# Performance work log

Measured on AMD Instinct MI355X. Metric: run time of the kernel, lower is better.

Reference implementation:

```python
import jax, jax.numpy as jnp
import numpy as np

NEG_INF = -1e9


def setup_inputs() -> dict:
    B, S, D = 4, 2048, 1024
    key = jax.random.key(0)
    ks = jax.random.split(key, 10)
    sc = 1.0 / np.sqrt(D)
    return {
        "batch": jax.random.normal(ks[0], (B, S, D), jnp.float32),
        "padding_mask": jax.random.randint(ks[1], (B, S), 0, 2) > 0,
        "Wq": jax.random.normal(ks[2], (D, D), jnp.float32) * sc,
        "bq": jnp.zeros((D,), jnp.float32),
        "Wk": jax.random.normal(ks[3], (D, D), jnp.float32) * sc,
        "bk": jnp.zeros((D,), jnp.float32),
        "Wv": jax.random.normal(ks[4], (D, D), jnp.float32) * sc,
        "bv": jnp.zeros((D,), jnp.float32),
        "Wo": jax.random.normal(ks[5], (D, D), jnp.float32) * sc,
        "bo": jnp.zeros((D,), jnp.float32),
        "num_heads": 16,
    }


def _split_heads(x, H):
    B, S, D = x.shape
    return x.reshape(B, S, H, D // H).transpose(0, 2, 1, 3)  # [B,H,S,hd]


def reference(batch, padding_mask, Wq, bq, Wk, bk, Wv, bv, Wo, bo, num_heads):
    B, S, D = batch.shape
    H = num_heads
    q = _split_heads(batch @ Wq + bq, H)  # [B,H,S,hd]
    k = _split_heads(batch @ Wk + bk, H)
    v = _split_heads(batch @ Wv + bv, H)
    # tf.keras.layers.Attention default: unscaled dot-product scores
    scores = jnp.einsum("bhqd,bhkd->bhqk", q, k)
    kmask = padding_mask[:, None, None, :]  # value/key mask -> masks score columns
    scores = jnp.where(kmask, scores, NEG_INF)
    probs = jax.nn.softmax(scores, axis=-1)
    ctx = jnp.einsum("bhqk,bhkd->bhqd", probs, v)
    # query mask zeroes padded query positions (tf Attention behavior)
    ctx = ctx * padding_mask[:, None, :, None].astype(ctx.dtype)
    ctx = ctx.transpose(0, 2, 1, 3).reshape(B, S, D)
    return ctx @ Wo + bo
```

## Files before the change

### kernel.cpp

```cpp
#include <hip/hip_runtime.h>


#define Bb 4
#define Ss 2048
#define Dd 1024
#define Hh 16
#define SZt 8388608

typedef short bf16x8 __attribute__((ext_vector_type(8)));
typedef _Float16 f16x8 __attribute__((ext_vector_type(8)));
typedef float f32x4 __attribute__((ext_vector_type(4)));
typedef float f32x16 __attribute__((ext_vector_type(16)));
typedef unsigned int u32x4 __attribute__((ext_vector_type(4)));
typedef unsigned short u16;

__device__ __forceinline__ float bf2f(u16 u) {
    return __builtin_bit_cast(float, ((unsigned)u) << 16);
}
__device__ __forceinline__ u16 f2bf(float f) {
    unsigned u = __builtin_bit_cast(unsigned, f);
    unsigned r = 0x7FFFu + ((u >> 16) & 1u);
    return (u16)((u + r) >> 16);
}
__device__ __forceinline__ u16 f2h(float f) {
    _Float16 h = (_Float16)f;
    return __builtin_bit_cast(u16, h);
}
__device__ __forceinline__ bf16x8 ldfrag(const u16* p) {
    return __builtin_bit_cast(bf16x8, *(const uint4*)p);
}
__device__ __forceinline__ f16x8 ldfragh(const u16* p) {
    return __builtin_bit_cast(f16x8, *(const uint4*)p);
}
__device__ __forceinline__ f32x4 mfma16h(f16x8 a, f16x8 b, f32x4 c) {
    return __builtin_amdgcn_mfma_f32_16x16x32_f16(a, b, c, 0, 0, 0);
}
__device__ __forceinline__ f32x16 mfma32(bf16x8 a, bf16x8 b, f32x16 c) {
    return __builtin_amdgcn_mfma_f32_32x32x16_bf16(a, b, c, 0, 0, 0);
}
__device__ __forceinline__ f32x16 mfma32h(f16x8 a, f16x8 b, f32x16 c) {
    return __builtin_amdgcn_mfma_f32_32x32x16_f16(a, b, c, 0, 0, 0);
}
__device__ __forceinline__ unsigned cvt_pk_bf16(float a, float b) {
    unsigned r;
    asm("v_cvt_pk_bf16_f32 %0, %1, %2" : "=v"(r) : "v"(a), "v"(b));
    return r;
}
__device__ __forceinline__ void gl2lds16(const u16* g, u16* l) {
    __builtin_amdgcn_global_load_lds(
        (const __attribute__((address_space(1))) u16*)g,
        (__attribute__((address_space(3))) u16*)l, 16, 0, 0);
}

__global__ void normalize_mask(const unsigned char* __restrict__ raw, float* __restrict__ out,
                               float* __restrict__ cnt, int n) {
    __shared__ int flags;
    __shared__ float scnt[Bb];
    if (threadIdx.x == 0) flags = 0;
    if (threadIdx.x < Bb) scnt[threadIdx.x] = 0.f;
    __syncthreads();
    int f = 0;
    for (int i = threadIdx.x; i < n; i += blockDim.x) {
        unsigned char c = raw[i];
        if ((i & 3) != 0 && c) f |= 1;
        if ((i & 3) == 1 && c >= 2) f |= 2;
        if ((i & 3) == 3 && c >= 2) f |= 4;
    }
    if (f) atomicOr(&flags, f);
    __syncthreads();
    int fl = flags;
    int layout;
    if (!(fl & 1)) layout = 0;
    else if (fl & 2) layout = 2;
    else if (fl & 4) layout = 3;
    else layout = 1;
    for (int i = threadIdx.x; i < n; i += blockDim.x) {
        int v;
        if (layout == 0)      v = ((const int*)raw)[i];
        else if (layout == 1) v = raw[i];
        else if (layout == 2) v = ((const u16*)raw)[i] != 0;
        else                  v = ((const unsigned*)raw)[i] != 0;
        out[i] = (v != 0) ? 1.0f : 0.0f;
        if (v == 0) atomicAdd(&scnt[i >> 11], 1.0f);
    }
    __syncthreads();
    if (threadIdx.x < Bb) cnt[threadIdx.x] = scnt[threadIdx.x];
}

__global__ void concat_bias(const float* __restrict__ a, const float* __restrict__ b,
                            const float* __restrict__ c, float* __restrict__ o) {
    int i = blockIdx.x * 256 + threadIdx.x;
    o[i] = (i < 1024) ? a[i] : ((i < 2048) ? b[i - 1024] : c[i - 2048]);
}

__global__ __launch_bounds__(256) void convert_xh(const float* __restrict__ X,
                                                  u16* __restrict__ Xh) {
    size_t i = ((size_t)blockIdx.x * 256 + threadIdx.x) * 4;
    float4 v = *(const float4*)(X + i);
    u16 h0 = f2h(v.x), h1 = f2h(v.y), h2 = f2h(v.z), h3 = f2h(v.w);
    uint2 ph = { (unsigned)h0 | ((unsigned)h1 << 16), (unsigned)h2 | ((unsigned)h3 << 16) };
    *(uint2*)(Xh + i) = ph;
}

__global__ __launch_bounds__(256) void transpose_wh(const float* __restrict__ W, u16* __restrict__ Wt) {
    __shared__ float t[32][33];
    const int tx = threadIdx.x, ty = threadIdx.y;
    const int n0 = blockIdx.x * 32, k0 = blockIdx.y * 32;
    #pragma unroll
    for (int i = 0; i < 4; i++)
        t[ty + i * 8][tx] = W[(size_t)(k0 + ty + i * 8) * Dd + n0 + tx];
    __syncthreads();
    #pragma unroll
    for (int i = 0; i < 4; i++)
        Wt[(size_t)(n0 + ty + i * 8) * Dd + k0 + tx] = f2h(t[tx][ty + i * 8]);
}
__global__ __launch_bounds__(256) void transpose_w(const float* __restrict__ W, u16* __restrict__ Wt) {
    __shared__ float t[32][33];
    const int tx = threadIdx.x, ty = threadIdx.y;
    const int n0 = blockIdx.x * 32, k0 = blockIdx.y * 32;
    #pragma unroll
    for (int i = 0; i < 4; i++)
        t[ty + i * 8][tx] = W[(size_t)(k0 + ty + i * 8) * Dd + n0 + tx];
    __syncthreads();
    #pragma unroll
    for (int i = 0; i < 4; i++)
        Wt[(size_t)(n0 + ty + i * 8) * Dd + k0 + tx] = f2bf(t[tx][ty + i * 8]);
}

__global__ __launch_bounds__(256) void gemm_qkv(
    const u16* __restrict__ Ah, const u16* __restrict__ Wcat, const float* __restrict__ bcat,
    const float* __restrict__ mnorm,
    u16* __restrict__ Qb, u16* __restrict__ Kb, u16* __restrict__ Vt)
{
    __shared__ u16 Ahs[128][64];
    __shared__ u16 Bs[128][64];
    const int tid = threadIdx.x, lane = tid & 63, wave = tid >> 6;
    const int wm = wave >> 1, wn = wave & 1;
    const int bm = blockIdx.y * 128, bn = blockIdx.x * 128;
    const bool isQ = (bn < 1024);
    const int l15 = lane & 15, lq = lane >> 4;
    const int sr = wave * 32 + (lane >> 3);
    const int sc = (lane & 7) * 8;
    const u16* agp = Ah + (size_t)(bm + sr) * Dd + sc;
    const u16* bgp = Wcat + (size_t)(bn + sr) * Dd + sc;

    f32x4 acc[4][4] = {};

    for (int k0 = 0; k0 < Dd; k0 += 64) {
        __syncthreads();
        #pragma unroll
        for (int j = 0; j < 4; j++) {
            gl2lds16(agp + k0 + (size_t)j * 8 * Dd, &Ahs[wave * 32 + j * 8][0]);
            gl2lds16(bgp + k0 + (size_t)j * 8 * Dd, &Bs[wave * 32 + j * 8][0]);
        }
        __syncthreads();
        #pragma unroll
        for (int kf = 0; kf < 2; kf++) {
            f16x8 b[4], a[4];
            #pragma unroll
            for (int nt = 0; nt < 4; nt++)
                b[nt] = ldfragh(&Bs[wn * 64 + nt * 16 + l15][kf * 32 + lq * 8]);
            #pragma unroll
            for (int mt = 0; mt < 4; mt++)
                a[mt] = ldfragh(&Ahs[wm * 64 + mt * 16 + l15][kf * 32 + lq * 8]);
            #pragma unroll
            for (int mt = 0; mt < 4; mt++)
                #pragma unroll
                for (int nt = 0; nt < 4; nt++)
                    acc[mt][nt] = mfma16h(a[mt], b[nt], acc[mt][nt]);
        }
    }
    const float LOG2E = 1.44269504088896f;
    float bv[4];
    #pragma unroll
    for (int nt = 0; nt < 4; nt++) bv[nt] = bcat[bn + wn * 64 + nt * 16 + l15];
    #pragma unroll
    for (int mt = 0; mt < 4; mt++) {
        int r0 = bm + wm * 64 + mt * 16 + lq * 4;
        float mk[4];
        if (!isQ) {
            #pragma unroll
            for (int rr = 0; rr < 4; rr++) mk[rr] = mnorm[r0 + rr];
        }
        #pragma unroll
        for (int nt = 0; nt < 4; nt++) {
            int col = bn + wn * 64 + nt * 16 + l15;
            if (col < 1024) {
                #pragma unroll
                for (int rr = 0; rr < 4; rr++)
                    Qb[(size_t)(r0 + rr) * Dd + col] = f2h((acc[mt][nt][rr] + bv[nt]) * LOG2E);
            } else if (col < 2048) {
                int c2 = col - 1024;
                #pragma unroll
                for (int rr = 0; rr < 4; rr++)
                    Kb[(size_t)(r0 + rr) * Dd + c2] = f2h((acc[mt][nt][rr] + bv[nt]) * mk[rr]);
            } else {
                int c2 = col - 2048;
                int hh = c2 >> 6, dd = c2 & 63, b_ = r0 >> 11, s0 = r0 & 2047;
                u16 e0 = f2bf((acc[mt][nt][0] + bv[nt]) * mk[0]);
                u16 e1 = f2bf((acc[mt][nt][1] + bv[nt]) * mk[1]);
                u16 e2 = f2bf((acc[mt][nt][2] + bv[nt]) * mk[2]);
                u16 e3 = f2bf((acc[mt][nt][3] + bv[nt]) * mk[3]);
                uint2 pk = { (unsigned)e0 | ((unsigned)e1 << 16), (unsigned)e2 | ((unsigned)e3 << 16) };
                *(uint2*)(Vt + (size_t)((b_ * Hh + hh) * 64 + dd) * Ss + s0) = pk;
            }
        }
    }
}

__global__ __launch_bounds__(256) void gemm_out(
    const u16* __restrict__ Ah, const u16* __restrict__ Wt,
    const float* __restrict__ bias, float* __restrict__ Cout)
{
    __shared__ u16 Ahs[128][64];
    __shared__ u16 Bs[128][64];
    const int tid = threadIdx.x, lane = tid & 63, wave = tid >> 6;
    const int wm = wave >> 1, wn = wave & 1;
    const int bm = blockIdx.y * 128, bn = blockIdx.x * 128;
    const int l15 = lane & 15, lq = lane >> 4;
    const int sr = wave * 32 + (lane >> 3);
    const int sc = (lane & 7) * 8;
    const u16* agp = Ah + (size_t)(bm + sr) * Dd + sc;
    const u16* bgp = Wt + (size_t)(bn + sr) * Dd + sc;

    f32x4 acc[4][4] = {};

    for (int k0 = 0; k0 < Dd; k0 += 64) {
        __syncthreads();
        #pragma unroll
        for (int j = 0; j < 4; j++) {
            gl2lds16(agp + k0 + (size_t)j * 8 * Dd, &Ahs[wave * 32 + j * 8][0]);
            gl2lds16(bgp + k0 + (size_t)j * 8 * Dd, &Bs[wave * 32 + j * 8][0]);
        }
        __syncthreads();
        #pragma unroll
        for (int kf = 0; kf < 2; kf++) {
            bf16x8 b[4], a[4];
            #pragma unroll
            for (int nt = 0; nt < 4; nt++)
                b[nt] = ldfrag(&Bs[wn * 64 + nt * 16 + l15][kf * 32 + lq * 8]);
            #pragma unroll
            for (int mt = 0; mt < 4; mt++)
                a[mt] = ldfrag(&Ahs[wm * 64 + mt * 16 + l15][kf * 32 + lq * 8]);
            #pragma unroll
            for (int mt = 0; mt < 4; mt++)
                #pragma unroll
                for (int nt = 0; nt < 4; nt++)
                    acc[mt][nt] = __builtin_amdgcn_mfma_f32_16x16x32_bf16(a[mt], b[nt], acc[mt][nt], 0, 0, 0);
        }
    }
    float bv[4];
    #pragma unroll
    for (int nt = 0; nt < 4; nt++) bv[nt] = bias[bn + wn * 64 + nt * 16 + l15];
    #pragma unroll
    for (int mt = 0; mt < 4; mt++) {
        int r0 = bm + wm * 64 + mt * 16 + lq * 4;
        #pragma unroll
        for (int nt = 0; nt < 4; nt++) {
            int col = bn + wn * 64 + nt * 16 + l15;
            #pragma unroll
            for (int rr = 0; rr < 4; rr++)
                Cout[(size_t)(r0 + rr) * Dd + col] = acc[mt][nt][rr] + bv[nt];
        }
    }
}

__global__ __launch_bounds__(512, 4) void attn_mfma(
    u16* qctx, const u16* __restrict__ Kb, const u16* __restrict__ Vt,
    const float* __restrict__ maskf, const float* __restrict__ cntp)
{
    __shared__ u16 Ks[64][72];
    __shared__ u16 Vs[64][72];
    __shared__ float li_s[8][32];
    const int tid = threadIdx.x, lane = tid & 63, wave = tid >> 6;
    const int l31 = lane & 31, hi = lane >> 5;
    const int bh = blockIdx.x, h = bh & 15, b = bh >> 4;
    const int q0 = blockIdx.y * 256;

    f16x8 qa[4];
    {
        const u16* qp = qctx + (size_t)(b * Ss + q0 + wave * 32 + l31) * Dd + h * 64 + hi * 8;
        #pragma unroll
        for (int kf = 0; kf < 4; kf++) qa[kf] = ldfragh(qp + kf * 16);
    }

    const int srow = tid >> 3, scol = (tid & 7) * 8;
    const u16* kgsrc = Kb + (size_t)(b * Ss + srow) * Dd + h * 64 + scol;
    const u16* vgsrc = Vt + (size_t)((b * Hh + h) * 64 + srow) * Ss + scol;
    u16* kdst = &Ks[srow][scol];
    u16* vdst = &Vs[srow][scol];

    f32x16 acc0 = {}, acc1 = {};
    float li = 0.f;

    uint4 kreg = *(const uint4*)kgsrc;
    uint4 vreg = *(const uint4*)vgsrc;

    for (int k0 = 0; k0 < Ss; k0 += 64) {
        __syncthreads();
        *(uint4*)kdst = kreg;
        *(uint4*)vdst = vreg;
        __syncthreads();
        int k0n = (k0 + 64 < Ss) ? k0 + 64 : 0;
        kreg = *(const uint4*)(kgsrc + (size_t)k0n * Dd);
        vreg = *(const uint4*)(vgsrc + k0n);

        #pragma unroll
        for (int nt = 0; nt < 2; nt++) {
            f32x16 sc = {};
            #pragma unroll
            for (int kf = 0; kf < 4; kf++) {
                f16x8 kb = ldfragh(&Ks[nt * 32 + l31][kf * 16 + hi * 8]);
                sc = mfma32h(kb, qa[kf], sc);
            }
            float p[16];
            #pragma unroll
            for (int r = 0; r < 8; r++) p[r] = __builtin_amdgcn_exp2f(sc[r]);
            li += ((p[0] + p[1]) + (p[2] + p[3])) + ((p[4] + p[5]) + (p[6] + p[7]));
            {
                unsigned w0 = cvt_pk_bf16(p[0], p[1]), w1 = cvt_pk_bf16(p[2], p[3]);
                unsigned w2 = cvt_pk_bf16(p[4], p[5]), w3 = cvt_pk_bf16(p[6], p[7]);
                auto s02 = __builtin_amdgcn_permlane32_swap((int)w0, (int)w2, false, false);
                auto s13 = __builtin_amdgcn_permlane32_swap((int)w1, (int)w3, false, false);
                u32x4 pw = { (unsigned)s02[0], (unsigned)s13[0], (unsigned)s02[1], (unsigned)s13[1] };
                bf16x8 pa0 = __builtin_bit_cast(bf16x8, pw);
                bf16x8 v00 = ldfrag(&Vs[l31][nt * 32 + hi * 8]);
                bf16x8 v10 = ldfrag(&Vs[32 + l31][nt * 32 + hi * 8]);
                acc0 = mfma32(pa0, v00, acc0);
                acc1 = mfma32(pa0, v10, acc1);
            }
            #pragma unroll
            for (int r = 8; r < 16; r++) p[r] = __builtin_amdgcn_exp2f(sc[r]);
            li += ((p[8] + p[9]) + (p[10] + p[11])) + ((p[12] + p[13]) + (p[14] + p[15]));
            {
                unsigned w4 = cvt_pk_bf16(p[8], p[9]),  w5 = cvt_pk_bf16(p[10], p[11]);
                unsigned w6 = cvt_pk_bf16(p[12], p[13]), w7 = cvt_pk_bf16(p[14], p[15]);
                auto s46 = __builtin_amdgcn_permlane32_swap((int)w4, (int)w6, false, false);
                auto s57 = __builtin_amdgcn_permlane32_swap((int)w5, (int)w7, false, false);
                u32x4 pw = { (unsigned)s46[0], (unsigned)s57[0], (unsigned)s46[1], (unsigned)s57[1] };
                bf16x8 pa1 = __builtin_bit_cast(bf16x8, pw);
                bf16x8 v01 = ldfrag(&Vs[l31][nt * 32 + 16 + hi * 8]);
                bf16x8 v11 = ldfrag(&Vs[32 + l31][nt * 32 + 16 + hi * 8]);
                acc0 = mfma32(pa1, v01, acc0);
                acc1 = mfma32(pa1, v11, acc1);
            }
        }
    }

    float li_tot = li + __shfl_xor(li, 32);
    if (hi == 0) li_s[wave][l31] = li_tot;
    __builtin_amdgcn_s_barrier();
    float cntb = cntp[b];
    #pragma unroll
    for (int g = 0; g < 4; g++) {
        float4 lv = *(const float4*)&li_s[wave][g * 8 + hi * 4];
        #pragma unroll
        for (int j = 0; j < 4; j++) {
            int r = g * 4 + j;
            int row = j + 8 * g + 4 * hi;
            int q = q0 + wave * 32 + row;
            float qm = maskf[b * Ss + q];
            float den = lv[j] - cntb;
            float rl = den > 0.f ? qm / den : 0.f;
            u16* op = qctx + (size_t)(b * Ss + q) * Dd + h * 64 + l31;
            op[0]  = f2bf(acc0[r] * rl);
            op[32] = f2bf(acc1[r] * rl);
        }
    }
}

extern "C" void kernel_launch(void* const* d_in, const int* in_sizes, int n_in,
                              void* d_out, int out_size, void* d_ws, size_t ws_size,
                              hipStream_t stream) {
    const float* X  = (const float*)d_in[0];
    const unsigned char* mr = (const unsigned char*)d_in[1];
    const float* Wq = (const float*)d_in[2];
    const float* bq = (const float*)d_in[3];
    const float* Wk = (const float*)d_in[4];
    const float* bk = (const float*)d_in[5];
    const float* Wv = (const float*)d_in[6];
    const float* bv = (const float*)d_in[7];
    const float* Wo = (const float*)d_in[8];
    const float* bo = (const float*)d_in[9];
    float* out = (float*)d_out;

    u16* wsb = (u16*)d_ws;
    u16* Xh  = wsb;
    u16* Qb  = wsb + (size_t)SZt;
    u16* Kb  = wsb + 2 * (size_t)SZt;
    u16* Vt  = wsb + 3 * (size_t)SZt;
    u16* Wot = Xh;
    u16* ob  = (u16*)d_out;
    u16* Wcat = ob + (size_t)SZt;
    u16* Wqt = Wcat;
    u16* Wkt = Wqt + 1048576;
    u16* Wvt = Wkt + 1048576;
    float* mnorm = (float*)(Wvt + 1048576);
    float* bcat  = mnorm + Bb * Ss;
    float* cntp  = bcat + 3072;

    dim3 tg(32, 32), tb(32, 8);

    normalize_mask<<<1, 1024, 0, stream>>>(mr, mnorm, cntp, Bb * Ss);
    concat_bias<<<12, 256, 0, stream>>>(bq, bk, bv, bcat);
    convert_xh<<<SZt / 1024, 256, 0, stream>>>(X, Xh);
    transpose_wh<<<tg, tb, 0, stream>>>(Wq, Wqt);
    transpose_wh<<<tg, tb, 0, stream>>>(Wk, Wkt);
    transpose_wh<<<tg, tb, 0, stream>>>(Wv, Wvt);
    gemm_qkv<<<dim3(24, 64), 256, 0, stream>>>(Xh, Wcat, bcat, mnorm, Qb, Kb, Vt);
    transpose_w<<<tg, tb, 0, stream>>>(Wo, Wot);
    attn_mfma<<<dim3(Bb * Hh, Ss / 256), 512, 0, stream>>>(Qb, Kb, Vt, mnorm, cntp);
    gemm_out<<<dim3(8, 64), 256, 0, stream>>>(Qb, Wot, bo, out);
}
```

Baseline: 311.0 us.

## Pipeline GEMM K-loop with multi-buffered LDS, swizzle, and 256-row tiles

Both projection GEMMs now use 512-thread blocks covering 256x128 output tiles. A is triple-buffered and B double-buffered in LDS, with global-to-LDS loads issued one or two k-steps ahead and partial vmcnt waits, so loads overlap MFMA work instead of serializing behind two syncthreads per step. LDS columns are XOR-swizzled by row to cut bank conflicts on fragment reads. The costs are more LDS per block, half as many blocks, and hand-placed waitcnt and barrier logic that depends on exact load counts.

```diff
diff --git a/kernel.cpp b/kernel.cpp
--- a/kernel.cpp
+++ b/kernel.cpp
@@ -34,6 +34,9 @@
 }
 __device__ __forceinline__ f32x4 mfma16h(f16x8 a, f16x8 b, f32x4 c) {
     return __builtin_amdgcn_mfma_f32_16x16x32_f16(a, b, c, 0, 0, 0);
+}
+__device__ __forceinline__ f32x4 mfma16b(bf16x8 a, bf16x8 b, f32x4 c) {
+    return __builtin_amdgcn_mfma_f32_16x16x32_bf16(a, b, c, 0, 0, 0);
 }
 __device__ __forceinline__ f32x16 mfma32(bf16x8 a, bf16x8 b, f32x16 c) {
     return __builtin_amdgcn_mfma_f32_32x32x16_bf16(a, b, c, 0, 0, 0);
@@ -127,49 +130,69 @@
         Wt[(size_t)(n0 + ty + i * 8) * Dd + k0 + tx] = f2bf(t[tx][ty + i * 8]);
 }
 
-__global__ __launch_bounds__(256) void gemm_qkv(
+__global__ __launch_bounds__(512, 2) void gemm_qkv(
     const u16* __restrict__ Ah, const u16* __restrict__ Wcat, const float* __restrict__ bcat,
     const float* __restrict__ mnorm,
     u16* __restrict__ Qb, u16* __restrict__ Kb, u16* __restrict__ Vt)
 {
-    __shared__ u16 Ahs[128][64];
-    __shared__ u16 Bs[128][64];
+    __shared__ u16 As[3][256][64];
+    __shared__ u16 Bs[2][128][64];
     const int tid = threadIdx.x, lane = tid & 63, wave = tid >> 6;
     const int wm = wave >> 1, wn = wave & 1;
-    const int bm = blockIdx.y * 128, bn = blockIdx.x * 128;
+    const int bm = blockIdx.y * 256, bn = blockIdx.x * 128;
     const bool isQ = (bn < 1024);
     const int l15 = lane & 15, lq = lane >> 4;
-    const int sr = wave * 32 + (lane >> 3);
-    const int sc = (lane & 7) * 8;
-    const u16* agp = Ah + (size_t)(bm + sr) * Dd + sc;
-    const u16* bgp = Wcat + (size_t)(bn + sr) * Dd + sc;
+    const int rl = lane >> 3;
+    const int s8 = ((lane & 7) ^ rl) * 8;
+    const u16* agp = Ah + (size_t)(bm + wave * 32 + rl) * Dd + s8;
+    const u16* bgp = Wcat + (size_t)(bn + wave * 16 + rl) * Dd + s8;
 
     f32x4 acc[4][4] = {};
 
-    for (int k0 = 0; k0 < Dd; k0 += 64) {
-        __syncthreads();
-        #pragma unroll
-        for (int j = 0; j < 4; j++) {
-            gl2lds16(agp + k0 + (size_t)j * 8 * Dd, &Ahs[wave * 32 + j * 8][0]);
-            gl2lds16(bgp + k0 + (size_t)j * 8 * Dd, &Bs[wave * 32 + j * 8][0]);
-        }
-        __syncthreads();
+    auto stageA = [&](int slot, int kt) {
+        u16* d = &As[slot][wave * 32][0];
+        const u16* g = agp + kt * 64;
+        #pragma unroll
+        for (int j = 0; j < 4; ++j)
+            gl2lds16(g + (size_t)(j * 8) * Dd, d + j * 8 * 64);
+    };
+    auto stageB = [&](int slot, int kt) {
+        u16* d = &Bs[slot][wave * 16][0];
+        const u16* g = bgp + kt * 64;
+        #pragma unroll
+        for (int j = 0; j < 2; ++j)
+            gl2lds16(g + (size_t)(j * 8) * Dd, d + j * 8 * 64);
+    };
+
+    stageA(0, 0); stageB(0, 0); stageA(1, 1);
+    asm volatile("s_waitcnt vmcnt(4)" ::: "memory");
+    __builtin_amdgcn_s_barrier();
+
+    int cs = 0;
+    for (int t = 0; t < 16; ++t) {
+        if (t < 15) stageB((t + 1) & 1, t + 1);
+        if (t < 14) { int ss = (cs >= 1) ? cs - 1 : cs + 2; stageA(ss, t + 2); }
         #pragma unroll
         for (int kf = 0; kf < 2; kf++) {
             f16x8 b[4], a[4];
             #pragma unroll
             for (int nt = 0; nt < 4; nt++)
-                b[nt] = ldfragh(&Bs[wn * 64 + nt * 16 + l15][kf * 32 + lq * 8]);
+                b[nt] = ldfragh(&Bs[t & 1][wn * 64 + nt * 16 + l15][(kf * 32 + lq * 8) ^ ((l15 & 7) * 8)]);
             #pragma unroll
             for (int mt = 0; mt < 4; mt++)
-                a[mt] = ldfragh(&Ahs[wm * 64 + mt * 16 + l15][kf * 32 + lq * 8]);
+                a[mt] = ldfragh(&As[cs][wm * 64 + mt * 16 + l15][(kf * 32 + lq * 8) ^ ((l15 & 7) * 8)]);
             #pragma unroll
             for (int mt = 0; mt < 4; mt++)
                 #pragma unroll
                 for (int nt = 0; nt < 4; nt++)
                     acc[mt][nt] = mfma16h(a[mt], b[nt], acc[mt][nt]);
         }
-    }
+        if (t < 14)       asm volatile("s_waitcnt vmcnt(4)" ::: "memory");
+        else if (t == 14) asm volatile("s_waitcnt vmcnt(0)" ::: "memory");
+        if (t < 15) __builtin_amdgcn_s_barrier();
+        cs = (cs >= 2) ? 0 : cs + 1;
+    }
+
     const float LOG2E = 1.44269504088896f;
     float bv[4];
     #pragma unroll
@@ -208,47 +231,67 @@
     }
 }
 
-__global__ __launch_bounds__(256) void gemm_out(
+__global__ __launch_bounds__(512, 2) void gemm_out(
     const u16* __restrict__ Ah, const u16* __restrict__ Wt,
     const float* __restrict__ bias, float* __restrict__ Cout)
 {
-    __shared__ u16 Ahs[128][64];
-    __shared__ u16 Bs[128][64];
+    __shared__ u16 As[3][256][64];
+    __shared__ u16 Bs[2][128][64];
     const int tid = threadIdx.x, lane = tid & 63, wave = tid >> 6;
     const int wm = wave >> 1, wn = wave & 1;
-    const int bm = blockIdx.y * 128, bn = blockIdx.x * 128;
+    const int bm = blockIdx.y * 256, bn = blockIdx.x * 128;
     const int l15 = lane & 15, lq = lane >> 4;
-    const int sr = wave * 32 + (lane >> 3);
-    const int sc = (lane & 7) * 8;
-    const u16* agp = Ah + (size_t)(bm + sr) * Dd + sc;
-    const u16* bgp = Wt + (size_t)(bn + sr) * Dd + sc;
+    const int rl = lane >> 3;
+    const int s8 = ((lane & 7) ^ rl) * 8;
+    const u16* agp = Ah + (size_t)(bm + wave * 32 + rl) * Dd + s8;
+    const u16* bgp = Wt + (size_t)(bn + wave * 16 + rl) * Dd + s8;
 
     f32x4 acc[4][4] = {};
 
-    for (int k0 = 0; k0 < Dd; k0 += 64) {
-        __syncthreads();
-        #pragma unroll
-        for (int j = 0; j < 4; j++) {
-            gl2lds16(agp + k0 + (size_t)j * 8 * Dd, &Ahs[wave * 32 + j * 8][0]);
-            gl2lds16(bgp + k0 + (size_t)j * 8 * Dd, &Bs[wave * 32 + j * 8][0]);
-        }
-        __syncthreads();
+    auto stageA = [&](int slot, int kt) {
+        u16* d = &As[slot][wave * 32][0];
+        const u16* g = agp + kt * 64;
+        #pragma unroll
+        for (int j = 0; j < 4; ++j)
+            gl2lds16(g + (size_t)(j * 8) * Dd, d + j * 8 * 64);
+    };
+    auto stageB = [&](int slot, int kt) {
+        u16* d = &Bs[slot][wave * 16][0];
+        const u16* g = bgp + kt * 64;
+        #pragma unroll
+        for (int j = 0; j < 2; ++j)
+            gl2lds16(g + (size_t)(j * 8) * Dd, d + j * 8 * 64);
+    };
+
+    stageA(0, 0); stageB(0, 0); stageA(1, 1);
+    asm volatile("s_waitcnt vmcnt(4)" ::: "memory");
+    __builtin_amdgcn_s_barrier();
+
+    int cs = 0;
+    for (int t = 0; t < 16; ++t) {
+        if (t < 15) stageB((t + 1) & 1, t + 1);
+        if (t < 14) { int ss = (cs >= 1) ? cs - 1 : cs + 2; stageA(ss, t + 2); }
         #pragma unroll
         for (int kf = 0; kf < 2; kf++) {
             bf16x8 b[4], a[4];
             #pragma unroll
             for (int nt = 0; nt < 4; nt++)
-                b[nt] = ldfrag(&Bs[wn * 64 + nt * 16 + l15][kf * 32 + lq * 8]);
+                b[nt] = ldfrag(&Bs[t & 1][wn * 64 + nt * 16 + l15][(kf * 32 + lq * 8) ^ ((l15 & 7) * 8)]);
             #pragma unroll
             for (int mt = 0; mt < 4; mt++)
-                a[mt] = ldfrag(&Ahs[wm * 64 + mt * 16 + l15][kf * 32 + lq * 8]);
+                a[mt] = ldfrag(&As[cs][wm * 64 + mt * 16 + l15][(kf * 32 + lq * 8) ^ ((l15 & 7) * 8)]);
             #pragma unroll
             for (int mt = 0; mt < 4; mt++)
                 #pragma unroll
                 for (int nt = 0; nt < 4; nt++)
-                    acc[mt][nt] = __builtin_amdgcn_mfma_f32_16x16x32_bf16(a[mt], b[nt], acc[mt][nt], 0, 0, 0);
-        }
-    }
+                    acc[mt][nt] = mfma16b(a[mt], b[nt], acc[mt][nt]);
+        }
+        if (t < 14)       asm volatile("s_waitcnt vmcnt(4)" ::: "memory");
+        else if (t == 14) asm volatile("s_waitcnt vmcnt(0)" ::: "memory");
+        if (t < 15) __builtin_amdgcn_s_barrier();
+        cs = (cs >= 2) ? 0 : cs + 1;
+    }
+
     float bv[4];
     #pragma unroll
     for (int nt = 0; nt < 4; nt++) bv[nt] = bias[bn + wn * 64 + nt * 16 + l15];
@@ -407,8 +450,8 @@
     transpose_wh<<<tg, tb, 0, stream>>>(Wq, Wqt);
     transpose_wh<<<tg, tb, 0, stream>>>(Wk, Wkt);
     transpose_wh<<<tg, tb, 0, stream>>>(Wv, Wvt);
-    gemm_qkv<<<dim3(24, 64), 256, 0, stream>>>(Xh, Wcat, bcat, mnorm, Qb, Kb, Vt);
+    gemm_qkv<<<dim3(24, 32), 512, 0, stream>>>(Xh, Wcat, bcat, mnorm, Qb, Kb, Vt);
     transpose_w<<<tg, tb, 0, stream>>>(Wo, Wot);
     attn_mfma<<<dim3(Bb * Hh, Ss / 256), 512, 0, stream>>>(Qb, Kb, Vt, mnorm, cntp);
-    gemm_out<<<dim3(8, 64), 256, 0, stream>>>(Qb, Wot, bo, out);
-}
+    gemm_out<<<dim3(8, 32), 512, 0, stream>>>(Qb, Wot, bo, out);
+}
```

New measurement: 293.8 us. 5.5% less time.
